# Kernel optimization log

Hardware: AMD Instinct MI355X
Metric: run time of the kernel (lower is better)

## Reference

```python
import jax, jax.numpy as jnp
import numpy as np

SIZE = 256

def _linear(x, W, b):
    # torch nn.Linear: y = x @ W^T + b, W has shape [out, in]
    return jnp.einsum('bsd,ed->bse', x, W) + b

def setup_inputs() -> dict:
    key = jax.random.key(0)
    ks = jax.random.split(key, 10)
    B, Sq, Sk, D = 8, 2048, 2048, SIZE
    s = 1.0 / np.sqrt(D)
    return {
        'x': jax.random.normal(ks[0], (B, Sq, D), jnp.float32),
        'states': jax.random.normal(ks[1], (B, Sk, D), jnp.float32),
        'Wq': jax.random.normal(ks[2], (D, D), jnp.float32) * s,
        'bq': jnp.zeros((D,), jnp.float32),
        'Wk': jax.random.normal(ks[3], (D, D), jnp.float32) * s,
        'bk': jnp.zeros((D,), jnp.float32),
        'Wv': jax.random.normal(ks[4], (D, D), jnp.float32) * s,
        'bv': jnp.zeros((D,), jnp.float32),
        'Wa': jax.random.normal(ks[5], (D, D), jnp.float32) * s,  # LuongAttention.fc
        'ba': jnp.zeros((D,), jnp.float32),
    }

def reference(x, states, Wq, bq, Wk, bk, Wv, bv, Wa, ba):
    q = _linear(x, Wq, bq)          # [B,Sq,D]
    k = _linear(states, Wk, bk)     # [B,Sk,D]
    v = _linear(states, Wv, bv)     # [B,Sk,D]
    wk = _linear(k, Wa, ba)         # [B,Sk,D]
    scores = jnp.einsum('bqd,bkd->bqk', q, wk)   # bmm(q, wk^T)
    scores = jax.nn.softmax(scores, axis=-1)
    # original: (v[:,None,:,:] * scores[...,None]).sum(-2) == matmul
    context = jnp.einsum('bqk,bkd->bqd', scores, v)
    return context
```

## Files before the change

kernel.cpp:

```cpp
#include <hip/hip_runtime.h>
#include <cstdint>
#include <cstddef>

typedef _Float16 half_t;
typedef _Float16 half8 __attribute__((ext_vector_type(8)));
typedef _Float16 half4v __attribute__((ext_vector_type(4)));
typedef float float4_ __attribute__((ext_vector_type(4)));

#define NB 8
#define SEQ 2048
#define DIM 256
#define NROWS (NB*SEQ)
#define KS 4
#define NIT 16

__device__ __forceinline__ void dma16(const half_t* g, half_t* l) {
    __builtin_amdgcn_global_load_lds(
        (const __attribute__((address_space(1))) void*)g,
        (__attribute__((address_space(3))) void*)l,
        16, 0, 0);
}

__global__ __launch_bounds__(256) void prep_kernel(
    const float* __restrict__ Wq, const float* __restrict__ Wk,
    const float* __restrict__ Wv, const float* __restrict__ Wa,
    const float* __restrict__ bq,
    half_t* __restrict__ M_hi, half_t* __restrict__ M_lo,
    half_t* __restrict__ Wk_hi, half_t* __restrict__ Wk_lo,
    half_t* __restrict__ Wv_hi, float* __restrict__ bq2)
{
    __shared__ float sWa[256];
    __shared__ float sred[256];
    const int d = blockIdx.x;
    const int m = threadIdx.x;
    sWa[m] = Wa[m * 256 + d];
    __syncthreads();

    const int idx = d * 256 + m;
    float a0 = 0.f, a1 = 0.f, a2 = 0.f, a3 = 0.f;
    #pragma unroll 8
    for (int e = 0; e < 256; e += 4) {
        a0 += sWa[e + 0] * Wq[(e + 0) * 256 + m];
        a1 += sWa[e + 1] * Wq[(e + 1) * 256 + m];
        a2 += sWa[e + 2] * Wq[(e + 2) * 256 + m];
        a3 += sWa[e + 3] * Wq[(e + 3) * 256 + m];
    }
    float acc = (a0 + a1) + (a2 + a3);
    half_t h = (half_t)acc;
    M_hi[idx] = h;
    M_lo[idx] = (half_t)(acc - (float)h);
    float wk = Wk[idx];
    h = (half_t)wk;
    Wk_hi[idx] = h;
    Wk_lo[idx] = (half_t)(wk - (float)h);
    Wv_hi[idx] = (half_t)Wv[idx];

    sred[m] = bq[m] * sWa[m];
    __syncthreads();
    #pragma unroll
    for (int s = 128; s > 0; s >>= 1) {
        if (m < s) sred[m] += sred[m + s];
        __syncthreads();
    }
    if (m == 0) bq2[d] = sred[0];
}

__global__ __launch_bounds__(256, 2) void linear_kernel(
    const float* __restrict__ x, const float* __restrict__ states,
    const half_t* __restrict__ M_hi, const half_t* __restrict__ M_lo, const float* __restrict__ bq2,
    const half_t* __restrict__ Wk_hi, const half_t* __restrict__ Wk_lo, const float* __restrict__ bk,
    const half_t* __restrict__ Wv_hi, const float* __restrict__ bv,
    half_t* __restrict__ q2_hi,
    half_t* __restrict__ k_hi,
    half_t* __restrict__ vT)
{
    __shared__ half_t sB[2 * 64 * 256];
    half_t* sBh = sB;
    half_t* sBl = sB + 64 * 256;

    const int seg  = blockIdx.x >> 8;
    const int t    = blockIdx.x & 255;
    const int tid  = threadIdx.x;
    const int lane = tid & 63;
    const int wv   = tid >> 6;
    const int quad = lane >> 4;
    const int l15  = lane & 15;
    const int rb   = t * 64;
    const int r0   = rb + wv * 16;

    const float* src  = (seg == 0) ? x : states;
    const half_t* Bh  = (seg == 0) ? M_hi : (seg == 1) ? Wk_hi : Wv_hi;
    const half_t* Bl  = (seg == 0) ? M_lo : Wk_lo;
    const float* bias = (seg == 0) ? bq2 : (seg == 1) ? bk : bv;

    half8 ah[8], al[8];
    #pragma unroll
    for (int c = 0; c < 8; ++c) {
        const float* pa = src + (size_t)(r0 + l15) * 256 + c * 32 + quad * 8;
        float4_ u0 = *(const float4_*)pa;
        float4_ u1 = *(const float4_*)(pa + 4);
        #pragma unroll
        for (int j = 0; j < 4; ++j) {
            half_t hh = (half_t)u0[j];
            ah[c][j] = hh; al[c][j] = (half_t)(u0[j] - (float)hh);
            hh = (half_t)u1[j];
            ah[c][4 + j] = hh; al[c][4 + j] = (half_t)(u1[j] - (float)hh);
        }
    }

    float4_ acc[16];
    if (seg != 2) {
        #pragma unroll
        for (int nt = 0; nt < 16; ++nt) {
            float be = bias[nt * 16 + l15];
            acc[nt] = {be, be, be, be};
        }
    } else {
        #pragma unroll
        for (int et = 0; et < 16; ++et)
            #pragma unroll
            for (int r = 0; r < 4; ++r)
                acc[et][r] = bias[et * 16 + quad * 4 + r];
    }

    #pragma unroll
    for (int eg = 0; eg < 4; ++eg) {
        __syncthreads();
        #pragma unroll
        for (int i = 0; i < 8; ++i) {
            int g = tid + i * 256;
            int e = g >> 5, c = g & 31;
            *(half8*)(sBh + e * 256 + ((c ^ (e & 7)) * 8)) =
                *(const half8*)(Bh + (size_t)(eg * 64 + e) * 256 + c * 8);
        }
        if (seg != 2) {
            #pragma unroll
            for (int i = 0; i < 8; ++i) {
                int g = tid + i * 256;
                int e = g >> 5, c = g & 31;
                *(half8*)(sBl + e * 256 + ((c ^ (e & 7)) * 8)) =
                    *(const half8*)(Bl + (size_t)(eg * 64 + e) * 256 + c * 8);
            }
        }
        __syncthreads();

        if (seg != 2) {
            #pragma unroll
            for (int ntl = 0; ntl < 4; ++ntl) {
                float4_ a = acc[eg * 4 + ntl];
                const int el = ntl * 16 + l15;
                #pragma unroll
                for (int c = 0; c < 8; ++c) {
                    int off = el * 256 + (((c * 4 + quad) ^ (el & 7)) * 8);
                    half8 bh = *(const half8*)(sBh + off);
                    half8 bl = *(const half8*)(sBl + off);
                    a = __builtin_amdgcn_mfma_f32_16x16x32_f16(ah[c], bh, a, 0, 0, 0);
                    a = __builtin_amdgcn_mfma_f32_16x16x32_f16(al[c], bh, a, 0, 0, 0);
                    a = __builtin_amdgcn_mfma_f32_16x16x32_f16(ah[c], bl, a, 0, 0, 0);
                }
                acc[eg * 4 + ntl] = a;
            }
        } else {
            #pragma unroll
            for (int ntl = 0; ntl < 4; ++ntl) {
                float4_ a = acc[eg * 4 + ntl];
                const int el = ntl * 16 + l15;
                #pragma unroll
                for (int c = 0; c < 8; ++c) {
                    int off = el * 256 + (((c * 4 + quad) ^ (el & 7)) * 8);
                    half8 aw = *(const half8*)(sBh + off);
                    a = __builtin_amdgcn_mfma_f32_16x16x32_f16(aw, ah[c], a, 0, 0, 0);
                }
                acc[eg * 4 + ntl] = a;
            }
        }
    }

    __syncthreads();
    if (seg != 2) {
        half_t* R = sB;
        #pragma unroll
        for (int nt = 0; nt < 16; ++nt)
            #pragma unroll
            for (int r = 0; r < 4; ++r)
                R[(wv * 16 + quad * 4 + r) * 256 + nt * 16 + l15] = (half_t)acc[nt][r];
        __syncthreads();
        if (seg == 0) {
            for (int i = 0; i < 8; ++i) {
                int g = tid + i * 256;
                int row = g >> 5, cc = g & 31;
                *(half8*)(q2_hi + (size_t)(rb + row) * 256 + cc * 8) =
                    *(const half8*)(R + row * 256 + cc * 8);
            }
        } else {
            for (int i = 0; i < 8; ++i) {
                int g = tid + i * 256;
                int row = g >> 5, cc = g & 31;
                int s = row & 31;
                size_t dst = ((size_t)(rb + row) >> 5) * 8192 + s * 256 + ((cc ^ (s & 7)) * 8);
                *(half8*)(k_hi + dst) = *(const half8*)(R + row * 256 + cc * 8);
            }
        }
    } else {
        half_t* sV = sB;
        #pragma unroll
        for (int et = 0; et < 16; ++et)
            #pragma unroll
            for (int r = 0; r < 4; ++r)
                sV[(et * 16 + quad * 4 + r) * 68 + wv * 16 + l15] = (half_t)acc[et][r];
        __syncthreads();
        const int b = rb >> 11, s0 = rb & 2047;
        for (int i = 0; i < 8; ++i) {
            int g = tid + i * 256;
            int d = g >> 3, sc8 = g & 7;
            int kt = (s0 >> 5) + (sc8 >> 2);
            int q  = sc8 & 3;
            int t32 = (sc8 >> 2) * 32;
            int slot = q ^ (d & 3) ^ ((d >> 2) & 3);
            half4v a4 = *(const half4v*)(sV + d * 68 + t32 + q * 4);
            half4v b4 = *(const half4v*)(sV + d * 68 + t32 + 16 + q * 4);
            half8 hv;
            hv[0] = a4[0]; hv[1] = a4[1]; hv[2] = a4[2]; hv[3] = a4[3];
            hv[4] = b4[0]; hv[5] = b4[1]; hv[6] = b4[2]; hv[7] = b4[3];
            size_t dst = ((size_t)b * 64 + kt) * 8192 + d * 32 + slot * 8;
            *(half8*)(vT + dst) = hv;
        }
    }
}

__global__ __launch_bounds__(256, 2) void attn_kernel(
    const half_t* __restrict__ q2_hi,
    const half_t* __restrict__ k_hi, const half_t* __restrict__ vT,
    half_t* __restrict__ pc, float* __restrict__ pm, float* __restrict__ pl)
{
    __shared__ __align__(16) unsigned char smem[64 * 1024];
    float* scr = (float*)smem;

    const int tid  = threadIdx.x;
    const int lane = tid & 63;
    const int wv   = tid >> 6;
    const int quad = lane >> 4;
    const int l15  = lane & 15;

    const int b  = blockIdx.x & 7;
    const int qt = (blockIdx.x >> 3) & 15;
    const int ks = blockIdx.x >> 7;

    const int qbase = b * 2048 + qt * 128 + wv * 32;

    half8 qf[2][8];
    #pragma unroll
    for (int ct = 0; ct < 2; ++ct)
        #pragma unroll
        for (int c = 0; c < 8; ++c)
            qf[ct][c] = *(const half8*)(q2_hi +
                (size_t)(qbase + ct * 16 + l15) * 256 + c * 32 + quad * 8);

    float4_ ctx[16][2];
    #pragma unroll
    for (int dt = 0; dt < 16; ++dt) {
        ctx[dt][0] = {0.f, 0.f, 0.f, 0.f};
        ctx[dt][1] = {0.f, 0.f, 0.f, 0.f};
    }
    float m_c[2] = {-1e30f, -1e30f};
    float l_c[2] = {0.f, 0.f};

    const half_t* kh_b = k_hi + (size_t)b * 64 * 8192;
    const half_t* vt_b = vT   + (size_t)b * 64 * 8192;
    const int t0 = ks * NIT;

    const int vslot8 = (quad ^ (l15 & 3) ^ ((l15 >> 2) & 3)) * 8;

    {
        const half_t* kt_ = kh_b + (size_t)t0 * 8192;
        #pragma unroll
        for (int i = 0; i < 4; ++i) {
            const int sg = i * 4 + wv;
            dma16(kt_ + sg * 512 + lane * 8, (half_t*)smem + sg * 512);
        }
        const half_t* vt_ = vt_b + (size_t)t0 * 8192;
        #pragma unroll
        for (int i = 0; i < 4; ++i) {
            const int sg = i * 4 + wv;
            dma16(vt_ + sg * 512 + lane * 8, (half_t*)(smem + 32768) + sg * 512);
        }
    }

    half8 pfp[2];
    #pragma unroll
    for (int ct = 0; ct < 2; ++ct)
        #pragma unroll
        for (int j = 0; j < 8; ++j) pfp[ct][j] = (half_t)0;

    for (int it = 0; it < NIT; ++it) {
        half_t* s_k  = (half_t*)(smem + ((it & 1) << 14));
        half_t* s_vP = (half_t*)(smem + 32768 + (((it + 1) & 1) << 14));
        const bool pre = (it + 1 < NIT);

        asm volatile("s_waitcnt vmcnt(4)" ::: "memory");
        __builtin_amdgcn_s_barrier();
        asm volatile("" ::: "memory");

        if (pre) {
            const half_t* kt_ = kh_b + (size_t)(t0 + it + 1) * 8192;
            half_t* kdst = (half_t*)(smem + (((it + 1) & 1) << 14));
            #pragma unroll
            for (int i = 0; i < 4; ++i) {
                const int sg = i * 4 + wv;
                dma16(kt_ + sg * 512 + lane * 8, kdst + sg * 512);
            }
        }

        float4_ S[2][2];
        S[0][0] = {0.f,0.f,0.f,0.f}; S[0][1] = {0.f,0.f,0.f,0.f};
        S[1][0] = {0.f,0.f,0.f,0.f}; S[1][1] = {0.f,0.f,0.f,0.f};
        __builtin_amdgcn_s_setprio(1);
        #pragma unroll
        for (int c = 0; c < 8; ++c) {
            #pragma unroll
            for (int kt = 0; kt < 2; ++kt) {
                const int key = kt * 16 + l15;
                const int off = key * 256 + (((c * 4 + quad) ^ (key & 7)) * 8);
                half8 kf = *(const half8*)(s_k + off);
                #pragma unroll
                for (int ct = 0; ct < 2; ++ct)
                    S[kt][ct] = __builtin_amdgcn_mfma_f32_16x16x32_f16(kf, qf[ct][c], S[kt][ct], 0, 0, 0);
            }
            if (it > 0) {
                #pragma unroll
                for (int dl = 0; dl < 2; ++dl) {
                    const int dt = c * 2 + dl;
                    half8 vf = *(const half8*)(s_vP + (dt * 16 + l15) * 32 + vslot8);
                    ctx[dt][0] = __builtin_amdgcn_mfma_f32_16x16x32_f16(vf, pfp[0], ctx[dt][0], 0, 0, 0);
                    ctx[dt][1] = __builtin_amdgcn_mfma_f32_16x16x32_f16(vf, pfp[1], ctx[dt][1], 0, 0, 0);
                }
            }
        }
        __builtin_amdgcn_s_setprio(0);
        __builtin_amdgcn_sched_barrier(0);
        __builtin_amdgcn_s_barrier();
        asm volatile("" ::: "memory");

        if (pre) {
            const half_t* vt_ = vt_b + (size_t)(t0 + it + 1) * 8192;
            half_t* vdst = (half_t*)(smem + 32768 + (((it + 1) & 1) << 14));
            #pragma unroll
            for (int i = 0; i < 4; ++i) {
                const int sg = i * 4 + wv;
                dma16(vt_ + sg * 512 + lane * 8, vdst + sg * 512);
            }
        }

        float mx0, mx1;
        {
            float a0 = fmaxf(fmaxf(S[0][0][0], S[0][0][1]), fmaxf(S[0][0][2], S[0][0][3]));
            float b0 = fmaxf(fmaxf(S[1][0][0], S[1][0][1]), fmaxf(S[1][0][2], S[1][0][3]));
            mx0 = fmaxf(a0, b0);
            float a1 = fmaxf(fmaxf(S[0][1][0], S[0][1][1]), fmaxf(S[0][1][2], S[0][1][3]));
            float b1 = fmaxf(fmaxf(S[1][1][0], S[1][1][1]), fmaxf(S[1][1][2], S[1][1][3]));
            mx1 = fmaxf(a1, b1);
        }
        const int doresc = __any((mx0 > m_c[0] + 8.f) || (mx1 > m_c[1] + 8.f));
        float alpha0 = 1.f, alpha1 = 1.f;
        if (doresc) {
            float r0 = fmaxf(mx0, __shfl_xor(mx0, 16));
            r0 = fmaxf(r0, __shfl_xor(r0, 32));
            float r1 = fmaxf(mx1, __shfl_xor(mx1, 16));
            r1 = fmaxf(r1, __shfl_xor(r1, 32));
            float mn0 = fmaxf(m_c[0], r0);
            float mn1 = fmaxf(m_c[1], r1);
            alpha0 = __expf(m_c[0] - mn0);
            alpha1 = __expf(m_c[1] - mn1);
            m_c[0] = mn0; m_c[1] = mn1;
        }
        half8 pfc[2];
        #pragma unroll
        for (int ct = 0; ct < 2; ++ct) {
            const float mm = m_c[ct];
            float rs = 0.f;
            #pragma unroll
            for (int r = 0; r < 4; ++r) {
                float p0 = __expf(S[0][ct][r] - mm);
                float p1 = __expf(S[1][ct][r] - mm);
                rs += p0 + p1;
                pfc[ct][r]     = (half_t)p0;
                pfc[ct][4 + r] = (half_t)p1;
            }
            l_c[ct] = l_c[ct] * (ct ? alpha1 : alpha0) + rs;
        }
        if (doresc) {
            #pragma unroll
            for (int dt = 0; dt < 16; ++dt)
                #pragma unroll
                for (int r = 0; r < 4; ++r) {
                    ctx[dt][0][r] *= alpha0;
                    ctx[dt][1][r] *= alpha1;
                }
        }
        pfp[0] = pfc[0];
        pfp[1] = pfc[1];
    }

    asm volatile("s_waitcnt vmcnt(0)" ::: "memory");
    __builtin_amdgcn_s_barrier();
    asm volatile("" ::: "memory");
    {
        half_t* s_v = (half_t*)(smem + 32768 + (((NIT - 1) & 1) << 14));
        __builtin_amdgcn_s_setprio(1);
        #pragma unroll
        for (int dt = 0; dt < 16; ++dt) {
            half8 vf = *(const half8*)(s_v + (dt * 16 + l15) * 32 + vslot8);
            ctx[dt][0] = __builtin_amdgcn_mfma_f32_16x16x32_f16(vf, pfp[0], ctx[dt][0], 0, 0, 0);
            ctx[dt][1] = __builtin_amdgcn_mfma_f32_16x16x32_f16(vf, pfp[1], ctx[dt][1], 0, 0, 0);
        }
        __builtin_amdgcn_s_setprio(0);
    }

    float lt[2];
    #pragma unroll
    for (int ct = 0; ct < 2; ++ct) {
        float s = l_c[ct];
        s += __shfl_xor(s, 16);
        s += __shfl_xor(s, 32);
        lt[ct] = s;
    }

    float rinv[2] = {1.0f / lt[0], 1.0f / lt[1]};
    float* sw = scr + wv * (32 * 68);
    half_t* pcs = pc + (size_t)ks * NROWS * 256;
    #pragma unroll
    for (int rd = 0; rd < 4; ++rd) {
        #pragma unroll
        for (int dtl = 0; dtl < 4; ++dtl) {
            const int dt = rd * 4 + dtl;
            #pragma unroll
            for (int ct = 0; ct < 2; ++ct)
                #pragma unroll
                for (int r = 0; r < 4; ++r)
                    sw[(ct * 16 + l15) * 68 + dtl * 16 + quad * 4 + r] = ctx[dt][ct][r] * rinv[ct];
        }
        #pragma unroll
        for (int i = 0; i < 8; ++i) {
            int g = lane + i * 64;
            int q = g >> 4, dc = g & 15;
            float4_ v4 = *(const float4_*)(sw + q * 68 + dc * 4);
            half4v h4;
            #pragma unroll
            for (int j = 0; j < 4; ++j) h4[j] = (half_t)v4[j];
            *(half4v*)(pcs + (size_t)(qbase + q) * 256 + rd * 64 + dc * 4) = h4;
        }
    }
    if (quad == 0) {
        #pragma unroll
        for (int ct = 0; ct < 2; ++ct) {
            const size_t row = qbase + ct * 16 + l15;
            pm[(size_t)ks * NROWS + row] = m_c[ct];
            pl[(size_t)ks * NROWS + row] = lt[ct];
        }
    }
}

__global__ __launch_bounds__(256) void combine_kernel(
    const half_t* __restrict__ pc, const float* __restrict__ pm,
    const float* __restrict__ pl, float* __restrict__ out)
{
    const int t = threadIdx.x;
    const int row = blockIdx.x * 4 + (t >> 6);
    const int d0 = (t & 63) * 4;
    float m[KS], l[KS];
    float ms = -1e30f;
    #pragma unroll
    for (int i = 0; i < KS; ++i) {
        m[i] = pm[(size_t)i * NROWS + row];
        l[i] = pl[(size_t)i * NROWS + row];
        ms = fmaxf(ms, m[i]);
    }
    float w[KS], tot = 0.f;
    #pragma unroll
    for (int i = 0; i < KS; ++i) {
        w[i] = l[i] * __expf(m[i] - ms);
        tot += w[i];
    }
    float inv = 1.0f / tot;
    float4_ o = {0.f, 0.f, 0.f, 0.f};
    #pragma unroll
    for (int i = 0; i < KS; ++i) {
        half4v y = *(const half4v*)(pc + ((size_t)i * NROWS + row) * 256 + d0);
        float wi = w[i] * inv;
        #pragma unroll
        for (int j = 0; j < 4; ++j) o[j] += wi * (float)y[j];
    }
    *(float4_*)(out + (size_t)row * 256 + d0) = o;
}

extern "C" void kernel_launch(void* const* d_in, const int* in_sizes, int n_in,
                              void* d_out, int out_size, void* d_ws, size_t ws_size,
                              hipStream_t stream) {
    const float* x      = (const float*)d_in[0];
    const float* states = (const float*)d_in[1];
    const float* Wq     = (const float*)d_in[2];
    const float* bq     = (const float*)d_in[3];
    const float* Wk     = (const float*)d_in[4];
    const float* bk     = (const float*)d_in[5];
    const float* Wv     = (const float*)d_in[6];
    const float* bv     = (const float*)d_in[7];
    const float* Wa     = (const float*)d_in[8];
    float* out = (float*)d_out;

    char* ws = (char*)d_ws;
    size_t off = 0;
    auto alloc = [&](size_t bytes) -> void* {
        void* p = ws + off;
        off += (bytes + 255) & ~(size_t)255;
        return p;
    };
    half_t* M_hi  = (half_t*)alloc(65536 * 2);
    half_t* M_lo  = (half_t*)alloc(65536 * 2);
    half_t* Wk_hi = (half_t*)alloc(65536 * 2);
    half_t* Wk_lo = (half_t*)alloc(65536 * 2);
    half_t* Wv_hi = (half_t*)alloc(65536 * 2);
    float*  bq2   = (float*)alloc(256 * 4);
    half_t* q2_hi = (half_t*)alloc((size_t)NROWS * 256 * 2);
    half_t* k_hi  = (half_t*)alloc((size_t)NROWS * 256 * 2);
    half_t* vT    = (half_t*)alloc((size_t)NROWS * 256 * 2);
    half_t* pc    = (half_t*)alloc((size_t)KS * NROWS * 256 * 2);
    float*  pm    = (float*)alloc((size_t)KS * NROWS * 4);
    float*  pl    = (float*)alloc((size_t)KS * NROWS * 4);

    prep_kernel<<<256, 256, 0, stream>>>(Wq, Wk, Wv, Wa, bq,
                                         M_hi, M_lo, Wk_hi, Wk_lo, Wv_hi, bq2);
    linear_kernel<<<768, 256, 0, stream>>>(x, states,
                                           M_hi, M_lo, bq2,
                                           Wk_hi, Wk_lo, bk,
                                           Wv_hi, bv,
                                           q2_hi, k_hi, vT);
    attn_kernel<<<8 * 16 * KS, 256, 0, stream>>>(q2_hi, k_hi, vT,
                                                 pc, pm, pl);
    combine_kernel<<<NROWS / 4, 256, 0, stream>>>(pc, pm, pl, out);
}
```

Before: 179.9 us.

## Fuse split-K combine into attention via tickets and DMA weight tiles to LDS

Removes the separate combine kernel. Each attention block bumps an atomic ticket for its (batch, q-tile), and the last of the KS split blocks merges the partial outputs into the final result. The prep kernel now writes the weight matrices pre-swizzled, so the linear kernel can load its weight tiles into LDS with global_load_lds DMA instead of register round-trips. This saves a kernel launch and some load instructions, but puts the merge work serially on the last block of each tile and adds fences and atomics.

```diff
diff --git a/kernel.cpp b/kernel.cpp
--- a/kernel.cpp
+++ b/kernel.cpp
@@ -27,16 +27,17 @@
     const float* __restrict__ bq,
     half_t* __restrict__ M_hi, half_t* __restrict__ M_lo,
     half_t* __restrict__ Wk_hi, half_t* __restrict__ Wk_lo,
-    half_t* __restrict__ Wv_hi, float* __restrict__ bq2)
+    half_t* __restrict__ Wv_hi, float* __restrict__ bq2,
+    int* __restrict__ tickets)
 {
     __shared__ float sWa[256];
     __shared__ float sred[256];
     const int d = blockIdx.x;
     const int m = threadIdx.x;
+    if (d == 0 && m < 128) tickets[m] = 0;
     sWa[m] = Wa[m * 256 + d];
     __syncthreads();
 
-    const int idx = d * 256 + m;
     float a0 = 0.f, a1 = 0.f, a2 = 0.f, a3 = 0.f;
     #pragma unroll 8
     for (int e = 0; e < 256; e += 4) {
@@ -46,14 +47,19 @@
         a3 += sWa[e + 3] * Wq[(e + 3) * 256 + m];
     }
     float acc = (a0 + a1) + (a2 + a3);
+
+    const int pos  = (((m >> 3) ^ (d & 7)) << 3) | (m & 7);
+    const int sidx = d * 256 + pos;
+    const int idx  = d * 256 + m;
+
     half_t h = (half_t)acc;
-    M_hi[idx] = h;
-    M_lo[idx] = (half_t)(acc - (float)h);
+    M_hi[sidx] = h;
+    M_lo[sidx] = (half_t)(acc - (float)h);
     float wk = Wk[idx];
     h = (half_t)wk;
-    Wk_hi[idx] = h;
-    Wk_lo[idx] = (half_t)(wk - (float)h);
-    Wv_hi[idx] = (half_t)Wv[idx];
+    Wk_hi[sidx] = h;
+    Wk_lo[sidx] = (half_t)(wk - (float)h);
+    Wv_hi[sidx] = (half_t)Wv[idx];
 
     sred[m] = bq[m] * sWa[m];
     __syncthreads();
@@ -126,20 +132,20 @@
     #pragma unroll
     for (int eg = 0; eg < 4; ++eg) {
         __syncthreads();
-        #pragma unroll
-        for (int i = 0; i < 8; ++i) {
-            int g = tid + i * 256;
-            int e = g >> 5, c = g & 31;
-            *(half8*)(sBh + e * 256 + ((c ^ (e & 7)) * 8)) =
-                *(const half8*)(Bh + (size_t)(eg * 64 + e) * 256 + c * 8);
-        }
-        if (seg != 2) {
+        {
+            const half_t* src_h = Bh + (size_t)eg * 16384;
             #pragma unroll
             for (int i = 0; i < 8; ++i) {
-                int g = tid + i * 256;
-                int e = g >> 5, c = g & 31;
-                *(half8*)(sBl + e * 256 + ((c ^ (e & 7)) * 8)) =
-                    *(const half8*)(Bl + (size_t)(eg * 64 + e) * 256 + c * 8);
+                const int sg = i * 4 + wv;
+                dma16(src_h + sg * 512 + lane * 8, sBh + sg * 512);
+            }
+            if (seg != 2) {
+                const half_t* src_l = Bl + (size_t)eg * 16384;
+                #pragma unroll
+                for (int i = 0; i < 8; ++i) {
+                    const int sg = i * 4 + wv;
+                    dma16(src_l + sg * 512 + lane * 8, sBl + sg * 512);
+                }
             }
         }
         __syncthreads();
@@ -231,9 +237,11 @@
 __global__ __launch_bounds__(256, 2) void attn_kernel(
     const half_t* __restrict__ q2_hi,
     const half_t* __restrict__ k_hi, const half_t* __restrict__ vT,
-    half_t* __restrict__ pc, float* __restrict__ pm, float* __restrict__ pl)
+    half_t* __restrict__ pc, float* __restrict__ pm, float* __restrict__ pl,
+    float* __restrict__ out, int* __restrict__ tickets)
 {
     __shared__ __align__(16) unsigned char smem[64 * 1024];
+    __shared__ int sLast;
     float* scr = (float*)smem;
 
     const int tid  = threadIdx.x;
@@ -458,39 +466,45 @@
             pl[(size_t)ks * NROWS + row] = lt[ct];
         }
     }
-}
-
-__global__ __launch_bounds__(256) void combine_kernel(
-    const half_t* __restrict__ pc, const float* __restrict__ pm,
-    const float* __restrict__ pl, float* __restrict__ out)
-{
-    const int t = threadIdx.x;
-    const int row = blockIdx.x * 4 + (t >> 6);
-    const int d0 = (t & 63) * 4;
-    float m[KS], l[KS];
-    float ms = -1e30f;
-    #pragma unroll
-    for (int i = 0; i < KS; ++i) {
-        m[i] = pm[(size_t)i * NROWS + row];
-        l[i] = pl[(size_t)i * NROWS + row];
-        ms = fmaxf(ms, m[i]);
-    }
-    float w[KS], tot = 0.f;
-    #pragma unroll
-    for (int i = 0; i < KS; ++i) {
-        w[i] = l[i] * __expf(m[i] - ms);
-        tot += w[i];
-    }
-    float inv = 1.0f / tot;
-    float4_ o = {0.f, 0.f, 0.f, 0.f};
-    #pragma unroll
-    for (int i = 0; i < KS; ++i) {
-        half4v y = *(const half4v*)(pc + ((size_t)i * NROWS + row) * 256 + d0);
-        float wi = w[i] * inv;
-        #pragma unroll
-        for (int j = 0; j < 4; ++j) o[j] += wi * (float)y[j];
-    }
-    *(float4_*)(out + (size_t)row * 256 + d0) = o;
+
+    __threadfence();
+    __syncthreads();
+    if (tid == 0)
+        sLast = (atomicAdd(&tickets[b * 16 + qt], 1) == KS - 1);
+    __syncthreads();
+    if (sLast) {
+        __threadfence();
+        const int rb0 = b * 2048 + qt * 128;
+        const int rlb = tid >> 6;
+        const int c4  = (tid & 63) * 4;
+        for (int i = 0; i < 32; ++i) {
+            const size_t row = rb0 + rlb + i * 4;
+            float mm[KS], ll[KS];
+            float ms = -1e30f;
+            #pragma unroll
+            for (int s = 0; s < KS; ++s) {
+                mm[s] = pm[(size_t)s * NROWS + row];
+                ll[s] = pl[(size_t)s * NROWS + row];
+                ms = fmaxf(ms, mm[s]);
+            }
+            float w[KS], tot = 0.f;
+            #pragma unroll
+            for (int s = 0; s < KS; ++s) {
+                w[s] = ll[s] * __expf(mm[s] - ms);
+                tot += w[s];
+            }
+            const float inv = 1.0f / tot;
+            float4_ o = {0.f, 0.f, 0.f, 0.f};
+            #pragma unroll
+            for (int s = 0; s < KS; ++s) {
+                half4v y = *(const half4v*)(pc + ((size_t)s * NROWS + row) * 256 + c4);
+                const float wi = w[s] * inv;
+                #pragma unroll
+                for (int j = 0; j < 4; ++j) o[j] += wi * (float)y[j];
+            }
+            *(float4_*)(out + row * 256 + c4) = o;
+        }
+    }
 }
 
 extern "C" void kernel_launch(void* const* d_in, const int* in_sizes, int n_in,
@@ -520,6 +534,7 @@
     half_t* Wk_lo = (half_t*)alloc(65536 * 2);
     half_t* Wv_hi = (half_t*)alloc(65536 * 2);
     float*  bq2   = (float*)alloc(256 * 4);
+    int*    tick  = (int*)alloc(512);
     half_t* q2_hi = (half_t*)alloc((size_t)NROWS * 256 * 2);
     half_t* k_hi  = (half_t*)alloc((size_t)NROWS * 256 * 2);
     half_t* vT    = (half_t*)alloc((size_t)NROWS * 256 * 2);
@@ -528,13 +543,13 @@
     float*  pl    = (float*)alloc((size_t)KS * NROWS * 4);
 
     prep_kernel<<<256, 256, 0, stream>>>(Wq, Wk, Wv, Wa, bq,
-                                         M_hi, M_lo, Wk_hi, Wk_lo, Wv_hi, bq2);
+                                         M_hi, M_lo, Wk_hi, Wk_lo, Wv_hi, bq2,
+                                         tick);
     linear_kernel<<<768, 256, 0, stream>>>(x, states,
                                            M_hi, M_lo, bq2,
                                            Wk_hi, Wk_lo, bk,
                                            Wv_hi, bv,
                                            q2_hi, k_hi, vT);
     attn_kernel<<<8 * 16 * KS, 256, 0, stream>>>(q2_hi, k_hi, vT,
-                                                 pc, pm, pl);
-    combine_kernel<<<NROWS / 4, 256, 0, stream>>>(pc, pm, pl, out);
+                                                 pc, pm, pl, out, tick);
 }
```

New measurement: 255.6 us. 1.42x slower.
